# Optimization experiments

Measured on AMD Instinct MI355X. Metric: run time of the kernel, lower is better.

## Reference

```python
import jax, jax.numpy as jnp
import numpy as np


def setup_inputs() -> dict:
    key = jax.random.key(0)
    ks = jax.random.split(key, 4)
    T, B, E = 2048, 2, 1024
    query = jax.random.normal(ks[0], (T, B, E), dtype=jnp.float32)
    attn_mask = jnp.zeros((T, T), dtype=jnp.float32)
    Wqkv = jax.random.normal(ks[1], (3 * E, E), dtype=jnp.float32) * 0.02
    bqkv = jnp.zeros((3 * E,), dtype=jnp.float32)
    Wout = jax.random.normal(ks[2], (E, E), dtype=jnp.float32) * 0.02
    bout = jnp.zeros((E,), dtype=jnp.float32)
    return {"query": query, "attn_mask": attn_mask, "Wqkv": Wqkv,
            "bqkv": bqkv, "Wout": Wout, "bout": bout, "num_heads": 16}


def reference(query, attn_mask, Wqkv, bqkv, Wout, bout, num_heads):
    T, B, E = query.shape
    H = num_heads
    hd = E // H
    scaling = hd ** -0.5
    # fused QKV projection: [T,B,3E]
    qkv = jnp.einsum('tbe,fe->tbf', query, Wqkv) + bqkv
    q, k, v = jnp.split(qkv, 3, axis=-1)
    q = q * scaling
    # [T,B,E] -> [B*H, T, hd]
    def to_heads(x):
        return x.reshape(T, B * H, hd).transpose(1, 0, 2)
    q, k, v = to_heads(q), to_heads(k), to_heads(v)
    # scores [B*H, T, T]
    scores = jnp.einsum('bth,bsh->bts', q, k) + attn_mask[None, :, :]
    probs = jax.nn.softmax(scores, axis=-1)  # dropout p=0
    attn = jnp.einsum('bts,bsh->bth', probs, v)  # [B*H, T, hd]
    attn = attn.transpose(1, 0, 2).reshape(T, B, E)
    out = jnp.einsum('tbe,fe->tbf', attn, Wout) + bout
    avg_w = probs.reshape(B, H, T, T).sum(axis=1) / H
    return out, avg_w
```

## Files before the change

kernel.cpp:

```cpp
#include <hip/hip_runtime.h>
#include <cstdint>
#include <cstddef>

#define Tt 2048
#define Bb 2
#define Ee 1024
#define Hh 16
#define HD 64
#define BHh (Bb*Hh)
#define Mm (Tt*Bb)

typedef short bf16x8 __attribute__((ext_vector_type(8)));
typedef float f32x4  __attribute__((ext_vector_type(4)));

#define MFMA16(a,b,c) __builtin_amdgcn_mfma_f32_16x16x32_bf16(a, b, c, 0, 0, 0)

__device__ __forceinline__ unsigned short f2bf(float f) {
    unsigned int u = __builtin_bit_cast(unsigned int, f);
    u += 0x7FFFu + ((u >> 16) & 1u);
    return (unsigned short)(u >> 16);
}
__device__ __forceinline__ unsigned int pack2bf(float lo, float hi) {
    return (unsigned int)f2bf(lo) | ((unsigned int)f2bf(hi) << 16);
}

__device__ __forceinline__ int swzA(int row, int dwcol) {
    return (row*32 + dwcol) ^ ((row & 7) << 2);
}
__device__ __forceinline__ int swzG(int row, int dwcol) {
    return (row*16 + dwcol) ^ ((row & 3) << 2);
}

__device__ __forceinline__ bf16x8 ldfrag(const unsigned short* base, int row, int col) {
    const unsigned int* p = (const unsigned int*)(base + row*66 + col);
    const unsigned int* q = (const unsigned int*)(base + row*66 + col + 16);
    uint4 u;
    u.x = p[0]; u.y = p[1];
    u.z = q[0]; u.w = q[1];
    return __builtin_bit_cast(bf16x8, u);
}

__global__ __launch_bounds__(256)
void to_bf16(const float* __restrict__ src, unsigned short* __restrict__ dst, int n8)
{
    const int stride = gridDim.x * 256;
    for (int i = blockIdx.x*256 + threadIdx.x; i < n8; i += stride) {
        const float4 a = ((const float4*)src)[2*i];
        const float4 b = ((const float4*)src)[2*i + 1];
        const uint4 u = {pack2bf(a.x,a.y), pack2bf(a.z,a.w),
                         pack2bf(b.x,b.y), pack2bf(b.z,b.w)};
        ((uint4*)dst)[i] = u;
    }
}

template<int MODE>
__global__ __launch_bounds__(256)
void gemm_mfma(const unsigned short* __restrict__ A, const unsigned short* __restrict__ W,
               const float* __restrict__ bias, float* __restrict__ Cout,
               unsigned short* __restrict__ qbuf, unsigned short* __restrict__ kbuf,
               unsigned short* __restrict__ vbuf, int N, int K)
{
    __shared__ __align__(16) unsigned int AsDW[128*16];
    __shared__ __align__(16) unsigned int WsDW[128*16];
    const int tid  = threadIdx.x;
    const int bm   = blockIdx.y * 128;
    const int bn   = blockIdx.x * 128;
    const int w    = tid >> 6;
    const int lane = tid & 63;
    const int lr   = lane & 15;
    const int lg   = lane >> 4;
    const int wm   = (w >> 1) * 64;
    const int wn   = (w & 1) * 64;

    f32x4 acc[4][4];
#pragma unroll
    for (int m = 0; m < 4; ++m)
#pragma unroll
        for (int n = 0; n < 4; ++n)
            acc[m][n] = f32x4{0.f, 0.f, 0.f, 0.f};

    const int r1  = tid >> 2;
    const int cdw = (tid & 3) * 4;

    for (int k0 = 0; k0 < K; k0 += 32) {
        __syncthreads();
        {
            const uint4 a0 = *(const uint4*)&A[(size_t)(bm + r1)      * K + k0 + cdw*2];
            const uint4 a1 = *(const uint4*)&A[(size_t)(bm + r1 + 64) * K + k0 + cdw*2];
            const uint4 w0 = *(const uint4*)&W[(size_t)(bn + r1)      * K + k0 + cdw*2];
            const uint4 w1 = *(const uint4*)&W[(size_t)(bn + r1 + 64) * K + k0 + cdw*2];
            *(uint4*)(AsDW + swzG(r1,      cdw)) = a0;
            *(uint4*)(AsDW + swzG(r1 + 64, cdw)) = a1;
            *(uint4*)(WsDW + swzG(r1,      cdw)) = w0;
            *(uint4*)(WsDW + swzG(r1 + 64, cdw)) = w1;
        }
        __syncthreads();

        bf16x8 af[4], wf[4];
#pragma unroll
        for (int i = 0; i < 4; ++i) {
            af[i] = __builtin_bit_cast(bf16x8, *(const uint4*)(AsDW + swzG(wm + 16*i + lr, 4*lg)));
            wf[i] = __builtin_bit_cast(bf16x8, *(const uint4*)(WsDW + swzG(wn + 16*i + lr, 4*lg)));
        }
#pragma unroll
        for (int m = 0; m < 4; ++m)
#pragma unroll
            for (int n = 0; n < 4; ++n)
                acc[m][n] = MFMA16(af[m], wf[n], acc[m][n]);
    }

#pragma unroll
    for (int nsub = 0; nsub < 4; ++nsub) {
        const int n0 = bn + wn + 16*nsub + lr;
        const float bv = bias[n0];
#pragma unroll
        for (int msub = 0; msub < 4; ++msub) {
#pragma unroll
            for (int reg = 0; reg < 4; ++reg) {
                const int m = bm + wm + 16*msub + 4*lg + reg;
                float v = acc[msub][nsub][reg] + bv;
                if (MODE == 0) {
                    const int which = n0 >> 10;
                    const int e0 = n0 & 1023;
                    const int h = e0 >> 6, d0 = e0 & 63;
                    if (which == 0) v *= 0.125f;
                    unsigned short* dst = (which == 0) ? qbuf : (which == 1) ? kbuf : vbuf;
                    dst[((size_t)((m & 1)*Hh + h) * Tt + (m >> 1)) * HD + d0] = f2bf(v);
                } else {
                    Cout[(size_t)m * N + n0] = v;
                }
            }
        }
    }
}

__global__ __launch_bounds__(512)
void attn_mfma(const unsigned short* __restrict__ qb, const unsigned short* __restrict__ kb,
               const unsigned short* __restrict__ vb, const float* __restrict__ mask,
               unsigned short* __restrict__ attnb, float* __restrict__ lbuf)
{
    __shared__ __align__(16) unsigned int KsDW[64*32];
    __shared__ __align__(16) unsigned short Vt[64][66];
    __shared__ float l_sh[128];

    const int tid  = threadIdx.x;
    const int bid  = blockIdx.x;
    const int wid  = (bid & 7) * 64 + (bid >> 3);
    const int bh   = wid & 31;
    const int t0   = (wid >> 5) * 128;
    const int w    = tid >> 6;
    const int lane = tid & 63;
    const int lr   = lane & 15;
    const int lg   = lane >> 4;
    const int b = bh >> 4, h = bh & 15;

    const unsigned short* __restrict__ Qg = qb + (size_t)bh * Tt * HD;
    const unsigned short* __restrict__ Kg = kb + (size_t)bh * Tt * HD;
    const unsigned short* __restrict__ Vg = vb + (size_t)bh * Tt * HD;

    const int str = tid >> 3;
    const int sdw = (tid & 7) * 4;

    const int vdg = tid & 15;
    const int vs2 = tid >> 4;

    bf16x8 qf[2];
    for (int half = 0; half < 2; ++half) {
        __syncthreads();
        *(uint4*)(KsDW + swzA(str, sdw)) =
            *(const uint4*)&Qg[(size_t)(t0 + half*64 + str) * HD + sdw*2];
        __syncthreads();
        if ((w >> 2) == half) {
            const int r = 16*(w & 3) + lr;
            qf[0] = __builtin_bit_cast(bf16x8, *(const uint4*)(KsDW + swzA(r, 4*lg)));
            qf[1] = __builtin_bit_cast(bf16x8, *(const uint4*)(KsDW + swzA(r, 16 + 4*lg)));
        }
    }

    f32x4 oacc[4];
#pragma unroll
    for (int d = 0; d < 4; ++d)
        oacc[d] = f32x4{0.f, 0.f, 0.f, 0.f};
    float lacc = 0.f;

    for (int s0 = 0; s0 < Tt; s0 += 64) {
        __syncthreads();
        *(uint4*)(KsDW + swzA(str, sdw)) =
            *(const uint4*)&Kg[(size_t)(s0 + str) * HD + sdw*2];
        {
            const uint2 a = *(const uint2*)&Vg[(size_t)(s0 + 2*vs2)     * HD + vdg*4];
            const uint2 c = *(const uint2*)&Vg[(size_t)(s0 + 2*vs2 + 1) * HD + vdg*4];
            *(unsigned int*)&Vt[vdg*4+0][2*vs2] = (a.x & 0xFFFFu) | (c.x << 16);
            *(unsigned int*)&Vt[vdg*4+1][2*vs2] = (a.x >> 16)     | (c.x & 0xFFFF0000u);
            *(unsigned int*)&Vt[vdg*4+2][2*vs2] = (a.y & 0xFFFFu) | (c.y << 16);
            *(unsigned int*)&Vt[vdg*4+3][2*vs2] = (a.y >> 16)     | (c.y & 0xFFFF0000u);
        }
        __syncthreads();

        f32x4 sacc[4];
#pragma unroll
        for (int ssub = 0; ssub < 4; ++ssub) {
            const bf16x8 a0 = __builtin_bit_cast(bf16x8,
                *(const uint4*)(KsDW + swzA(16*ssub + lr, 4*lg)));
            const bf16x8 a1 = __builtin_bit_cast(bf16x8,
                *(const uint4*)(KsDW + swzA(16*ssub + lr, 16 + 4*lg)));
            f32x4 z = {0.f, 0.f, 0.f, 0.f};
            z = MFMA16(a0, qf[0], z);
            z = MFMA16(a1, qf[1], z);
            sacc[ssub] = z;
        }

        unsigned int pw[8];
        {
            float lt = 0.f;
            const float* __restrict__ mrow =
                &mask[(size_t)(t0 + 16*w + lr) * Tt + s0];
#pragma unroll
            for (int ssub = 0; ssub < 4; ++ssub) {
                const float4 mv = *(const float4*)&mrow[16*ssub + 4*lg];
                const float e0 = __expf(sacc[ssub][0] + mv.x);
                const float e1 = __expf(sacc[ssub][1] + mv.y);
                const float e2 = __expf(sacc[ssub][2] + mv.z);
                const float e3 = __expf(sacc[ssub][3] + mv.w);
                lt += (e0 + e1) + (e2 + e3);
                pw[ssub*2]     = pack2bf(e0, e1);
                pw[ssub*2 + 1] = pack2bf(e2, e3);
            }
            lt += __shfl_xor(lt, 16);
            lt += __shfl_xor(lt, 32);
            lacc += lt;
        }

        const uint4 ua = {pw[0], pw[1], pw[2], pw[3]};
        const uint4 ub = {pw[4], pw[5], pw[6], pw[7]};
#pragma unroll
        for (int dsub = 0; dsub < 4; ++dsub) {
            const bf16x8 b0 = ldfrag(&Vt[0][0], 16*dsub + lr, 4*lg);
            const bf16x8 b1 = ldfrag(&Vt[0][0], 16*dsub + lr, 32 + 4*lg);
            oacc[dsub] = MFMA16(__builtin_bit_cast(bf16x8, ua), b0, oacc[dsub]);
            oacc[dsub] = MFMA16(__builtin_bit_cast(bf16x8, ub), b1, oacc[dsub]);
        }
    }

    __syncthreads();
    if (lg == 0) l_sh[16*w + lr] = lacc;
    __syncthreads();
#pragma unroll
    for (int reg = 0; reg < 4; ++reg) {
        const int tl = 16*w + 4*lg + reg;
        const float inv = 1.f / l_sh[tl];
        const int t = t0 + tl;
#pragma unroll
        for (int dsub = 0; dsub < 4; ++dsub)
            attnb[((size_t)t * Bb + b) * Ee + h*HD + dsub*16 + lr] =
                f2bf(oacc[dsub][reg] * inv);
    }
    if (lg == 0)
        lbuf[(size_t)bh * Tt + t0 + 16*w + lr] = lacc;
}

__global__ __launch_bounds__(256)
void avg_probs_mfma(const unsigned short* __restrict__ qb, const unsigned short* __restrict__ kb,
                    const float* __restrict__ mask, const float* __restrict__ lbuf,
                    float* __restrict__ avg)
{
    __shared__ unsigned short Qs[64][66];
    __shared__ unsigned short Ksh[64][66];
    __shared__ float linv[16][64];

    const int tid  = threadIdx.x;
    const int b    = blockIdx.z;
    const int t0   = blockIdx.y * 64;
    const int s0   = blockIdx.x * 64;
    const int w    = tid >> 6;
    const int lane = tid & 63;
    const int lr   = lane & 15;
    const int lg   = lane >> 4;

    {
        const int h = tid >> 4, tl = (tid & 15) * 4;
        const float4 lv = *(const float4*)&lbuf[(size_t)(b*Hh + h) * Tt + t0 + tl];
        linv[h][tl+0] = 1.f / (16.f * lv.x);
        linv[h][tl+1] = 1.f / (16.f * lv.y);
        linv[h][tl+2] = 1.f / (16.f * lv.z);
        linv[h][tl+3] = 1.f / (16.f * lv.w);
    }

    f32x4 mf[4];
#pragma unroll
    for (int ssub = 0; ssub < 4; ++ssub)
#pragma unroll
        for (int reg = 0; reg < 4; ++reg)
            mf[ssub][reg] = mask[(size_t)(t0 + 16*w + 4*lg + reg) * Tt + s0 + 16*ssub + lr];

    f32x4 av[4];
#pragma unroll
    for (int ssub = 0; ssub < 4; ++ssub) av[ssub] = f32x4{0.f, 0.f, 0.f, 0.f};

    const int str = tid >> 2;
    const int stc = (tid & 3) * 16;

    for (int h = 0; h < Hh; ++h) {
        const unsigned short* __restrict__ Qg = qb + (size_t)(b*Hh + h) * Tt * HD;
        const unsigned short* __restrict__ Kg = kb + (size_t)(b*Hh + h) * Tt * HD;
        __syncthreads();
        {
            const unsigned short* Qp = &Qg[(size_t)(t0 + str) * HD + stc];
            const unsigned short* Kp = &Kg[(size_t)(s0 + str) * HD + stc];
            const uint4 q0 = *(const uint4*)Qp;
            const uint4 q1 = *(const uint4*)(Qp + 8);
            const uint4 k0 = *(const uint4*)Kp;
            const uint4 k1 = *(const uint4*)(Kp + 8);
            *(uint4*)&Qs[str][stc]      = q0;
            *(uint4*)&Qs[str][stc + 8]  = q1;
            *(uint4*)&Ksh[str][stc]     = k0;
            *(uint4*)&Ksh[str][stc + 8] = k1;
        }
        __syncthreads();

        const float lv0 = linv[h][16*w + 4*lg + 0];
        const float lv1 = linv[h][16*w + 4*lg + 1];
        const float lv2 = linv[h][16*w + 4*lg + 2];
        const float lv3 = linv[h][16*w + 4*lg + 3];

        const bf16x8 af0 = ldfrag(&Qs[0][0], 16*w + lr, 4*lg);
        const bf16x8 af1 = ldfrag(&Qs[0][0], 16*w + lr, 32 + 4*lg);
#pragma unroll
        for (int ssub = 0; ssub < 4; ++ssub) {
            const bf16x8 bf0 = ldfrag(&Ksh[0][0], 16*ssub + lr, 4*lg);
            const bf16x8 bf1 = ldfrag(&Ksh[0][0], 16*ssub + lr, 32 + 4*lg);
            f32x4 z = {0.f, 0.f, 0.f, 0.f};
            z = MFMA16(af0, bf0, z);
            z = MFMA16(af1, bf1, z);
            av[ssub][0] += __expf(z[0] + mf[ssub][0]) * lv0;
            av[ssub][1] += __expf(z[1] + mf[ssub][1]) * lv1;
            av[ssub][2] += __expf(z[2] + mf[ssub][2]) * lv2;
            av[ssub][3] += __expf(z[3] + mf[ssub][3]) * lv3;
        }
    }

#pragma unroll
    for (int ssub = 0; ssub < 4; ++ssub)
#pragma unroll
        for (int reg = 0; reg < 4; ++reg)
            avg[((size_t)b * Tt + t0 + 16*w + 4*lg + reg) * Tt + s0 + 16*ssub + lr] =
                av[ssub][reg];
}

extern "C" void kernel_launch(void* const* d_in, const int* in_sizes, int n_in,
                              void* d_out, int out_size, void* d_ws, size_t ws_size,
                              hipStream_t stream)
{
    (void)in_sizes; (void)n_in; (void)out_size; (void)ws_size;
    const float* query = (const float*)d_in[0];
    const float* mask  = (const float*)d_in[1];
    const float* Wqkv  = (const float*)d_in[2];
    const float* bqkv  = (const float*)d_in[3];
    const float* Wout  = (const float*)d_in[4];
    const float* bout  = (const float*)d_in[5];

    float* out = (float*)d_out;
    float* avg = out + (size_t)Tt * Bb * Ee;

    const size_t S1 = (size_t)BHh * Tt * HD;
    unsigned short* wsu     = (unsigned short*)d_ws;
    unsigned short* qbuf    = wsu;
    unsigned short* kbuf    = qbuf + S1;
    unsigned short* vbuf    = kbuf + S1;
    unsigned short* attnb   = vbuf + S1;
    unsigned short* querybf = attnb + (size_t)Mm * Ee;
    unsigned short* wqkvbf  = querybf + (size_t)Mm * Ee;
    unsigned short* woutbf  = wqkvbf + (size_t)3 * Ee * Ee;
    float*          lbuf    = (float*)(woutbf + (size_t)Ee * Ee);

    to_bf16<<<1024, 256, 0, stream>>>(query, querybf, (Mm*Ee)/8);
    to_bf16<<<1024, 256, 0, stream>>>(Wqkv, wqkvbf, (3*Ee*Ee)/8);
    to_bf16<<<512,  256, 0, stream>>>(Wout, woutbf, (Ee*Ee)/8);

    gemm_mfma<0><<<dim3(3072/128, Mm/128), 256, 0, stream>>>(
        querybf, wqkvbf, bqkv, nullptr, qbuf, kbuf, vbuf, 3072, Ee);
    attn_mfma<<<dim3(BHh * (Tt/128)), 512, 0, stream>>>(
        qbuf, kbuf, vbuf, mask, attnb, lbuf);
    avg_probs_mfma<<<dim3(Tt/64, Tt/64, Bb), 256, 0, stream>>>(
        qbuf, kbuf, mask, lbuf, avg);
    gemm_mfma<1><<<dim3(Ee/128, Mm/128), 256, 0, stream>>>(
        attnb, woutbf, bout, out, nullptr, nullptr, nullptr, Ee, Ee);
}
```

Baseline: 224.2 us.

## Double-buffer K/V tiles in attention kernel with register prefetch

The attention loop now keeps two LDS buffers for K and transposed V. The next tile's global loads are issued into registers before the current tile's MFMA work and written to the other buffer afterwards. This hides global memory latency behind compute and cuts the loop from two barriers to one per iteration. The cost is twice the shared memory per block and more live registers, which may lower occupancy.

Result: faster. 213.7 us (-4.7%).

```diff
diff --git a/kernel.cpp b/kernel.cpp
--- a/kernel.cpp
+++ b/kernel.cpp
@@ -139,8 +139,8 @@
                const unsigned short* __restrict__ vb, const float* __restrict__ mask,
                unsigned short* __restrict__ attnb, float* __restrict__ lbuf)
 {
-    __shared__ __align__(16) unsigned int KsDW[64*32];
-    __shared__ __align__(16) unsigned short Vt[64][66];
+    __shared__ __align__(16) unsigned int KsDW[2][64*32];
+    __shared__ __align__(16) unsigned short Vt[2][64*66];
     __shared__ float l_sh[128];
 
     const int tid  = threadIdx.x;
@@ -167,13 +167,13 @@
     bf16x8 qf[2];
     for (int half = 0; half < 2; ++half) {
         __syncthreads();
-        *(uint4*)(KsDW + swzA(str, sdw)) =
+        *(uint4*)(KsDW[0] + swzA(str, sdw)) =
             *(const uint4*)&Qg[(size_t)(t0 + half*64 + str) * HD + sdw*2];
         __syncthreads();
         if ((w >> 2) == half) {
             const int r = 16*(w & 3) + lr;
-            qf[0] = __builtin_bit_cast(bf16x8, *(const uint4*)(KsDW + swzA(r, 4*lg)));
-            qf[1] = __builtin_bit_cast(bf16x8, *(const uint4*)(KsDW + swzA(r, 16 + 4*lg)));
+            qf[0] = __builtin_bit_cast(bf16x8, *(const uint4*)(KsDW[0] + swzA(r, 4*lg)));
+            qf[1] = __builtin_bit_cast(bf16x8, *(const uint4*)(KsDW[0] + swzA(r, 16 + 4*lg)));
         }
     }
 
@@ -183,27 +183,40 @@
         oacc[d] = f32x4{0.f, 0.f, 0.f, 0.f};
     float lacc = 0.f;
 
+    {
+        const uint4 k0r = *(const uint4*)&Kg[(size_t)str * HD + sdw*2];
+        const uint2 a0  = *(const uint2*)&Vg[(size_t)(2*vs2)     * HD + vdg*4];
+        const uint2 c0  = *(const uint2*)&Vg[(size_t)(2*vs2 + 1) * HD + vdg*4];
+        __syncthreads();
+        *(uint4*)(KsDW[0] + swzA(str, sdw)) = k0r;
+        unsigned short* vt0 = &Vt[0][0];
+        *(unsigned int*)&vt0[(vdg*4+0)*66 + 2*vs2] = (a0.x & 0xFFFFu) | (c0.x << 16);
+        *(unsigned int*)&vt0[(vdg*4+1)*66 + 2*vs2] = (a0.x >> 16)     | (c0.x & 0xFFFF0000u);
+        *(unsigned int*)&vt0[(vdg*4+2)*66 + 2*vs2] = (a0.y & 0xFFFFu) | (c0.y << 16);
+        *(unsigned int*)&vt0[(vdg*4+3)*66 + 2*vs2] = (a0.y >> 16)     | (c0.y & 0xFFFF0000u);
+        __syncthreads();
+    }
+
+    int cur = 0;
     for (int s0 = 0; s0 < Tt; s0 += 64) {
-        __syncthreads();
-        *(uint4*)(KsDW + swzA(str, sdw)) =
-            *(const uint4*)&Kg[(size_t)(s0 + str) * HD + sdw*2];
-        {
-            const uint2 a = *(const uint2*)&Vg[(size_t)(s0 + 2*vs2)     * HD + vdg*4];
-            const uint2 c = *(const uint2*)&Vg[(size_t)(s0 + 2*vs2 + 1) * HD + vdg*4];
-            *(unsigned int*)&Vt[vdg*4+0][2*vs2] = (a.x & 0xFFFFu) | (c.x << 16);
-            *(unsigned int*)&Vt[vdg*4+1][2*vs2] = (a.x >> 16)     | (c.x & 0xFFFF0000u);
-            *(unsigned int*)&Vt[vdg*4+2][2*vs2] = (a.y & 0xFFFFu) | (c.y << 16);
-            *(unsigned int*)&Vt[vdg*4+3][2*vs2] = (a.y >> 16)     | (c.y & 0xFFFF0000u);
-        }
-        __syncthreads();
+        const bool has_next = (s0 + 64 < Tt);
+        uint4 kn; uint2 van, vcn;
+        if (has_next) {
+            kn  = *(const uint4*)&Kg[(size_t)(s0 + 64 + str) * HD + sdw*2];
+            van = *(const uint2*)&Vg[(size_t)(s0 + 64 + 2*vs2)     * HD + vdg*4];
+            vcn = *(const uint2*)&Vg[(size_t)(s0 + 64 + 2*vs2 + 1) * HD + vdg*4];
+        }
+
+        const unsigned int* Kc = KsDW[cur];
+        const unsigned short* Vc = &Vt[cur][0];
 
         f32x4 sacc[4];
 #pragma unroll
         for (int ssub = 0; ssub < 4; ++ssub) {
             const bf16x8 a0 = __builtin_bit_cast(bf16x8,
-                *(const uint4*)(KsDW + swzA(16*ssub + lr, 4*lg)));
+                *(const uint4*)(Kc + swzA(16*ssub + lr, 4*lg)));
             const bf16x8 a1 = __builtin_bit_cast(bf16x8,
-                *(const uint4*)(KsDW + swzA(16*ssub + lr, 16 + 4*lg)));
+                *(const uint4*)(Kc + swzA(16*ssub + lr, 16 + 4*lg)));
             f32x4 z = {0.f, 0.f, 0.f, 0.f};
             z = MFMA16(a0, qf[0], z);
             z = MFMA16(a1, qf[1], z);
@@ -235,14 +248,24 @@
         const uint4 ub = {pw[4], pw[5], pw[6], pw[7]};
 #pragma unroll
         for (int dsub = 0; dsub < 4; ++dsub) {
-            const bf16x8 b0 = ldfrag(&Vt[0][0], 16*dsub + lr, 4*lg);
-            const bf16x8 b1 = ldfrag(&Vt[0][0], 16*dsub + lr, 32 + 4*lg);
+            const bf16x8 b0 = ldfrag(Vc, 16*dsub + lr, 4*lg);
+            const bf16x8 b1 = ldfrag(Vc, 16*dsub + lr, 32 + 4*lg);
             oacc[dsub] = MFMA16(__builtin_bit_cast(bf16x8, ua), b0, oacc[dsub]);
             oacc[dsub] = MFMA16(__builtin_bit_cast(bf16x8, ub), b1, oacc[dsub]);
         }
-    }
-
-    __syncthreads();
+
+        if (has_next) {
+            *(uint4*)(KsDW[cur ^ 1] + swzA(str, sdw)) = kn;
+            unsigned short* vt1 = &Vt[cur ^ 1][0];
+            *(unsigned int*)&vt1[(vdg*4+0)*66 + 2*vs2] = (van.x & 0xFFFFu) | (vcn.x << 16);
+            *(unsigned int*)&vt1[(vdg*4+1)*66 + 2*vs2] = (van.x >> 16)     | (vcn.x & 0xFFFF0000u);
+            *(unsigned int*)&vt1[(vdg*4+2)*66 + 2*vs2] = (van.y & 0xFFFFu) | (vcn.y << 16);
+            *(unsigned int*)&vt1[(vdg*4+3)*66 + 2*vs2] = (van.y >> 16)     | (vcn.y & 0xFFFF0000u);
+        }
+        __syncthreads();
+        cur ^= 1;
+    }
+
     if (lg == 0) l_sh[16*w + lr] = lacc;
     __syncthreads();
 #pragma unroll
```
